# Optimization experiments

Measured on AMD Instinct MI355X. Metric: run time of the kernel, lower is better.

Reference implementation:

```python
import jax, jax.numpy as jnp
import numpy as np
import math

B, T, C, H = 2, 2048, 1024, 16


def setup_inputs() -> dict:
    key = jax.random.key(0)
    k1, k2, k3 = jax.random.split(key, 3)
    x = jax.random.normal(k1, (B, T, C), dtype=jnp.float32)
    qkv_w = jax.random.normal(k2, (3 * C, C), dtype=jnp.float32) * 0.02
    proj_w = jax.random.normal(k3, (C, C), dtype=jnp.float32) * 0.02
    distance_scales = jnp.full((H,), 0.1, dtype=jnp.float32)
    return {"x": x, "qkv_w": qkv_w, "proj_w": proj_w, "distance_scales": distance_scales}


def reference(x, qkv_w, proj_w, distance_scales):
    b, t, c = x.shape
    h = distance_scales.shape[0]
    dh = c // h
    scale = 1.0 / math.sqrt(dh)

    # torch Linear: y = x @ W^T ; split into q, k, v
    qkv = jnp.einsum('btc,oc->bto', x, qkv_w)  # [B,T,3C]
    q, k, v = jnp.split(qkv, 3, axis=-1)
    q = q.reshape(b, t, h, dh).transpose(0, 2, 1, 3)  # [B,H,T,Dh]
    k = k.reshape(b, t, h, dh).transpose(0, 2, 1, 3)
    v = v.reshape(b, t, h, dh).transpose(0, 2, 1, 3)

    logits = jnp.einsum('bhid,bhjd->bhij', q, k) * scale  # [B,H,T,T]

    idx = jnp.arange(t)
    dists = jnp.abs(idx[:, None] - idx[None, :]).astype(x.dtype)  # [T,T]
    logits = logits - distance_scales[None, :, None, None] * dists

    causal = idx[None, :] > idx[:, None]  # True above diagonal -> masked
    logits = jnp.where(causal[None, None, :, :], -jnp.inf, logits)

    attn = jax.nn.softmax(logits, axis=-1)  # [B,H,T,T]

    dist_energy = (attn * dists).sum(axis=-1).mean()
    flop_energy = -(attn * jnp.log(attn + 1e-9)).sum(axis=-1).mean()

    out = jnp.einsum('bhij,bhjd->bhid', attn, v)  # [B,H,T,Dh]
    out = out.transpose(0, 2, 1, 3).reshape(b, t, c)
    out = jnp.einsum('btc,oc->bto', out, proj_w)

    return (out, dist_energy, flop_energy, jax.lax.stop_gradient(attn), jax.lax.stop_gradient(dists))
```

## Files before the change

kernel.cpp:

```cpp
#include <hip/hip_runtime.h>
#include <hip/hip_bf16.h>
#include <math.h>

#define T_SEQ 2048
#define C3 3072
#define C_DIM 1024

typedef __bf16 bf16_t;
typedef __bf16 bf16x8 __attribute__((ext_vector_type(8)));
typedef __bf16 bf16x4_t __attribute__((ext_vector_type(4)));
typedef float f32x4 __attribute__((ext_vector_type(4)));

typedef __attribute__((address_space(1))) const void gconst_t;
typedef __attribute__((address_space(3))) void lds_t;

static __device__ __forceinline__ bf16x8 ldg8(const bf16_t* p) {
    return *reinterpret_cast<const bf16x8*>(p);
}

__global__ void cvt4_kernel(const float* __restrict__ in, bf16_t* __restrict__ out,
                            long n4, float* zbuf) {
    long i = (long)blockIdx.x * blockDim.x + threadIdx.x;
    if (zbuf && i < 2) zbuf[i] = 0.f;
    long stride = (long)gridDim.x * blockDim.x;
    for (; i < n4; i += stride) {
        float4 v = ((const float4*)in)[i];
        bf16x4_t o;
        o[0] = (bf16_t)v.x; o[1] = (bf16_t)v.y; o[2] = (bf16_t)v.z; o[3] = (bf16_t)v.w;
        *(bf16x4_t*)(out + i * 4) = o;
    }
}

__global__ void dists_kernel(float* __restrict__ dout) {
    int idx = blockIdx.x * 256 + threadIdx.x;
    int i = idx >> 11, j = idx & 2047;
    dout[idx] = (float)(i > j ? i - j : j - i);
}

template <int BM, bool OUT_BF16>
__global__ __launch_bounds__(256) void gemm_bt(const bf16_t* __restrict__ A,
                                               const bf16_t* __restrict__ Bw,
                                               void* __restrict__ Cout,
                                               int M, int N, int K) {
    constexpr int WM = BM / 2;
    constexpr int MI = WM / 16;
    __shared__ bf16_t sA[BM * 64];
    __shared__ bf16_t sB[128 * 64];
    int tid = threadIdx.x, lane = tid & 63, wid = tid >> 6;
    int m = lane & 15, quad = lane >> 4;
    int wm = (wid >> 1) * WM, wn = (wid & 1) * 64;
    int m0 = blockIdx.y * BM, n0 = blockIdx.x * 128;
    int lrow = lane >> 3, cxor = (lane & 7) ^ (lrow & 7);

    const bf16_t* Ag = A + (size_t)(m0 + wid * 8 + lrow) * K + cxor * 8;
    const bf16_t* Bg = Bw + (size_t)(n0 + wid * 8 + lrow) * K + cxor * 8;

    f32x4 acc[MI][4] = {};
    for (int k0 = 0; k0 < K; k0 += 64) {
        for (int p = 0; p < BM / 32; ++p)
            __builtin_amdgcn_global_load_lds((gconst_t*)(Ag + (size_t)(p * 32) * K + k0),
                                             (lds_t*)(sA + (p * 32 + wid * 8) * 64), 16, 0, 0);
        for (int p = 0; p < 4; ++p)
            __builtin_amdgcn_global_load_lds((gconst_t*)(Bg + (size_t)(p * 32) * K + k0),
                                             (lds_t*)(sB + (p * 32 + wid * 8) * 64), 16, 0, 0);
        __syncthreads();
        for (int ks = 0; ks < 2; ++ks) {
            bf16x8 a[MI], b[4];
            for (int i = 0; i < MI; ++i) {
                int r = wm + i * 16 + m;
                a[i] = *(const bf16x8*)(sA + r * 64 + ((((ks << 2) + quad) ^ (r & 7)) << 3));
            }
            for (int j = 0; j < 4; ++j) {
                int r = wn + j * 16 + m;
                b[j] = *(const bf16x8*)(sB + r * 64 + ((((ks << 2) + quad) ^ (r & 7)) << 3));
            }
            for (int i = 0; i < MI; ++i)
                for (int j = 0; j < 4; ++j)
                    acc[i][j] = __builtin_amdgcn_mfma_f32_16x16x32_bf16(b[j], a[i], acc[i][j], 0, 0, 0);
        }
        __syncthreads();
    }
    for (int i = 0; i < MI; ++i)
        for (int j = 0; j < 4; ++j) {
            size_t row = m0 + wm + i * 16 + m;
            int col = n0 + wn + j * 16 + quad * 4;
            if (OUT_BF16) {
                bf16x4_t o;
                for (int r = 0; r < 4; ++r) o[r] = (bf16_t)acc[i][j][r];
                *(bf16x4_t*)((bf16_t*)Cout + row * N + col) = o;
            } else {
                *(f32x4*)((float*)Cout + row * N + col) = acc[i][j];
            }
        }
}

__global__ __launch_bounds__(256) void repack_vt(const bf16_t* __restrict__ qkv,
                                                 bf16_t* __restrict__ vt) {
    __shared__ bf16_t s[64][72];
    int t0 = (blockIdx.x & 31) << 6;
    int bh = blockIdx.x >> 5;
    int b = bh >> 4, h = bh & 15;
    int tid = threadIdx.x;
    int r = tid >> 3, c8 = (tid & 7) << 3;
    const bf16_t* src = qkv + (size_t)(b * T_SEQ) * C3 + 2048 + h * 64;
    for (int p = 0; p < 2; ++p) {
        int t = r + p * 32;
        *(uint4*)&s[t][c8] = *(const uint4*)&src[(size_t)(t0 + t) * C3 + c8];
    }
    __syncthreads();
    bf16_t* dst = vt + (size_t)bh * 64 * T_SEQ;
    for (int p = 0; p < 2; ++p) {
        int d = r + p * 32;
        bf16x8 vv;
        for (int i = 0; i < 8; ++i) vv[i] = s[c8 + i][d];
        *(bf16x8*)&dst[(size_t)d * T_SEQ + t0 + c8] = vv;
    }
}

__global__ __launch_bounds__(256) void attn_kernel(const bf16_t* __restrict__ qkv,
                                                   const bf16_t* __restrict__ vt,
                                                   const float* __restrict__ dscales,
                                                   float* __restrict__ attn,
                                                   bf16_t* __restrict__ y,
                                                   float* __restrict__ ews) {
    __shared__ bf16_t sP[64][72];
    __shared__ float sred[8];
    int base = blockIdx.x & 31;
    int bh = blockIdx.x >> 5;
    int it = (bh & 8) ? (31 - base) : base;
    int b = bh >> 4, h = bh & 15;
    int i0 = it << 6;
    int tid = threadIdx.x, lane = tid & 63, wid = tid >> 6;
    int m = lane & 15, quad = lane >> 4;
    int w16 = wid << 4;
    float dsc = dscales[h];
    const float scale = 0.125f;
    const float zthr = 111.0f;

    const bf16_t* Qb = qkv + (size_t)(b * T_SEQ) * C3 + h * 64;
    const bf16_t* Kb = Qb + 1024;
    const bf16_t* Vb = vt + (size_t)bh * 64 * T_SEQ;
    float* Ab = attn + ((size_t)bh * T_SEQ + i0) * T_SEQ;

    {
        int zc0 = i0 + 64, zn = T_SEQ - zc0;
        f32x4 z4 = {0.f, 0.f, 0.f, 0.f};
        for (int r = 0; r < 64; ++r) {
            float* rowp = Ab + (size_t)r * T_SEQ + zc0;
            for (int c = tid << 2; c < zn; c += 1024)
                *(f32x4*)(rowp + c) = z4;
        }
    }

    int i = i0 + w16 + m;
    bf16x8 qf[2];
    qf[0] = ldg8(Qb + (size_t)i * C3 + quad * 8);
    qf[1] = ldg8(Qb + (size_t)i * C3 + 32 + quad * 8);

    float lsum = 0.f;
    for (int jt = 0; jt <= it; ++jt) {
        int j0 = jt << 6;
        if ((float)(i0 - j0 - 63) * dsc > zthr) continue;
        f32x4 acc[4] = {};
        for (int ks = 0; ks < 2; ++ks)
            for (int n = 0; n < 4; ++n) {
                bf16x8 kf = ldg8(Kb + (size_t)(j0 + n * 16 + m) * C3 + ks * 32 + quad * 8);
                acc[n] = __builtin_amdgcn_mfma_f32_16x16x32_bf16(kf, qf[ks], acc[n], 0, 0, 0);
            }
        if (jt < it) {
            for (int n = 0; n < 4; ++n)
                for (int r = 0; r < 4; ++r) {
                    float d = (float)(i - (j0 + n * 16 + quad * 4 + r));
                    lsum += __expf(acc[n][r] * scale - dsc * d);
                }
        } else {
            for (int n = 0; n < 4; ++n)
                for (int r = 0; r < 4; ++r) {
                    int j = j0 + n * 16 + quad * 4 + r;
                    if (j <= i) lsum += __expf(acc[n][r] * scale - dsc * (float)(i - j));
                }
        }
    }
    lsum += __shfl_xor(lsum, 16);
    lsum += __shfl_xor(lsum, 32);
    float rl = 1.f / lsum;

    f32x4 oacc[4] = {};
    float e_d = 0.f, e_e = 0.f;

    for (int jt = 0; jt <= it; ++jt) {
        int j0 = jt << 6;
        if ((float)(i0 - j0 - 63) * dsc > zthr) {
            int rr = tid >> 2, c0 = (tid & 3) << 4;
            float* p0 = Ab + (size_t)rr * T_SEQ + j0 + c0;
            f32x4 z4 = {0.f, 0.f, 0.f, 0.f};
            for (int u = 0; u < 4; ++u) *(f32x4*)(p0 + u * 4) = z4;
            continue;
        }
        f32x4 acc[4] = {};
        for (int ks = 0; ks < 2; ++ks)
            for (int n = 0; n < 4; ++n) {
                bf16x8 kf = ldg8(Kb + (size_t)(j0 + n * 16 + m) * C3 + ks * 32 + quad * 8);
                acc[n] = __builtin_amdgcn_mfma_f32_16x16x32_bf16(kf, qf[ks], acc[n], 0, 0, 0);
            }
        __syncthreads();
        bool diag = (jt == it);
        for (int n = 0; n < 4; ++n) {
            f32x4 pv;
            for (int r = 0; r < 4; ++r) {
                int j = j0 + n * 16 + quad * 4 + r;
                float p = 0.f;
                if (!diag || j <= i) {
                    float d = (float)(i - j);
                    p = __expf(acc[n][r] * scale - dsc * d) * rl;
                    e_d += p * d;
                    e_e += p * __logf(p + 1e-9f);
                }
                pv[r] = p;
            }
            *(f32x4*)(Ab + (size_t)(w16 + m) * T_SEQ + j0 + n * 16 + quad * 4) = pv;
            bf16x4_t pb;
            for (int r = 0; r < 4; ++r) pb[r] = (bf16_t)pv[r];
            *(bf16x4_t*)&sP[w16 + m][n * 16 + quad * 4] = pb;
        }
        __syncthreads();
        for (int ks = 0; ks < 2; ++ks) {
            bf16x8 pf = *(const bf16x8*)&sP[w16 + m][ks * 32 + quad * 8];
            for (int n = 0; n < 4; ++n) {
                bf16x8 vf = ldg8(Vb + (size_t)(n * 16 + m) * T_SEQ + j0 + ks * 32 + quad * 8);
                oacc[n] = __builtin_amdgcn_mfma_f32_16x16x32_bf16(vf, pf, oacc[n], 0, 0, 0);
            }
        }
    }

    for (int n = 0; n < 4; ++n) {
        bf16x4_t o;
        for (int r = 0; r < 4; ++r) o[r] = (bf16_t)oacc[n][r];
        *(bf16x4_t*)(y + (size_t)(b * T_SEQ + i) * C_DIM + h * 64 + n * 16 + quad * 4) = o;
    }

    for (int off = 1; off < 64; off <<= 1) {
        e_d += __shfl_xor(e_d, off);
        e_e += __shfl_xor(e_e, off);
    }
    if (lane == 0) { sred[wid] = e_d; sred[wid + 4] = e_e; }
    __syncthreads();
    if (tid == 0) {
        atomicAdd(ews, sred[0] + sred[1] + sred[2] + sred[3]);
        atomicAdd(ews + 1, sred[4] + sred[5] + sred[6] + sred[7]);
    }
}

__global__ void finalize_kernel(const float* __restrict__ ews, float* __restrict__ dout) {
    dout[4194304] = ews[0] / 65536.f;
    dout[4194305] = -ews[1] / 65536.f;
}

extern "C" void kernel_launch(void* const* d_in, const int* in_sizes, int n_in,
                              void* d_out, int out_size, void* d_ws, size_t ws_size,
                              hipStream_t stream) {
    const float* x = (const float*)d_in[0];
    const float* qkv_w = (const float*)d_in[1];
    const float* proj_w = (const float*)d_in[2];
    const float* dscales = (const float*)d_in[3];
    float* out = (float*)d_out;

    char* ws = (char*)d_ws;
    float* ews   = (float*)ws;
    bf16_t* xb   = (bf16_t*)(ws + 256);
    bf16_t* wb   = xb + 4194304;
    bf16_t* pb   = wb + 3145728;
    bf16_t* qkvb = pb + 1048576;
    bf16_t* vtb  = qkvb + 12582912;
    bf16_t* yb   = vtb + 4194304;

    cvt4_kernel<<<1024, 256, 0, stream>>>(x, xb, 4194304 / 4, ews);
    cvt4_kernel<<<1024, 256, 0, stream>>>(qkv_w, wb, 3145728 / 4, nullptr);
    cvt4_kernel<<<512, 256, 0, stream>>>(proj_w, pb, 1048576 / 4, nullptr);
    dists_kernel<<<16384, 256, 0, stream>>>(out + 138412034);

    gemm_bt<128, true><<<dim3(24, 32), 256, 0, stream>>>(xb, wb, qkvb, 4096, 3072, 1024);
    repack_vt<<<1024, 256, 0, stream>>>(qkvb, vtb);
    attn_kernel<<<1024, 256, 0, stream>>>(qkvb, vtb, dscales, out + 4194306, yb, ews);
    gemm_bt<64, false><<<dim3(8, 64), 256, 0, stream>>>(yb, pb, out, 4096, 1024, 1024);
    finalize_kernel<<<1, 1, 0, stream>>>(ews, out);
}
```

Measured before the change: 873.2 us.

## Fuse prep kernels, tighten distance skip, use nontemporal stores and cheaper entropy

Merges the three fp32-to-bf16 conversion launches and the distance-matrix launch into one kernel. In attention, computes a start tile from the distance scale so that tiles whose probabilities underflow are never visited; their region is bulk-zeroed instead. All attention-matrix and zero writes become nontemporal stores. Entropy is computed as sum p*logit minus log of the row sum, removing a log per element. The tighter threshold drops contributions below roughly exp(-38), which slightly changes numerics.

```diff
diff --git a/kernel.cpp b/kernel.cpp
--- a/kernel.cpp
+++ b/kernel.cpp
@@ -18,23 +18,38 @@
     return *reinterpret_cast<const bf16x8*>(p);
 }
 
-__global__ void cvt4_kernel(const float* __restrict__ in, bf16_t* __restrict__ out,
-                            long n4, float* zbuf) {
-    long i = (long)blockIdx.x * blockDim.x + threadIdx.x;
-    if (zbuf && i < 2) zbuf[i] = 0.f;
-    long stride = (long)gridDim.x * blockDim.x;
-    for (; i < n4; i += stride) {
-        float4 v = ((const float4*)in)[i];
-        bf16x4_t o;
-        o[0] = (bf16_t)v.x; o[1] = (bf16_t)v.y; o[2] = (bf16_t)v.z; o[3] = (bf16_t)v.w;
-        *(bf16x4_t*)(out + i * 4) = o;
-    }
-}
-
-__global__ void dists_kernel(float* __restrict__ dout) {
-    int idx = blockIdx.x * 256 + threadIdx.x;
-    int i = idx >> 11, j = idx & 2047;
-    dout[idx] = (float)(i > j ? i - j : j - i);
+__global__ __launch_bounds__(256) void aux_kernel(const float* __restrict__ x,
+                                                  const float* __restrict__ qw,
+                                                  const float* __restrict__ pw,
+                                                  bf16_t* __restrict__ xb,
+                                                  bf16_t* __restrict__ wb,
+                                                  bf16_t* __restrict__ pb,
+                                                  float* __restrict__ dout,
+                                                  float* __restrict__ ews) {
+    long gid = (long)blockIdx.x * 256 + threadIdx.x;
+    if (gid < 2) ews[gid] = 0.f;
+    const float* src;
+    bf16_t* dst;
+    long u;
+    if (gid < 1048576) { src = x; dst = xb; u = gid; }
+    else if (gid < 1835008) { src = qw; dst = wb; u = gid - 1048576; }
+    else if (gid < 2097152) { src = pw; dst = pb; u = gid - 1835008; }
+    else {
+        long v = gid - 2097152;
+        long e0 = v << 2;
+        int i = (int)(e0 >> 11), j0 = (int)(e0 & 2047);
+        f32x4 o;
+        for (int r = 0; r < 4; ++r) {
+            int j = j0 + r;
+            o[r] = (float)(i > j ? i - j : j - i);
+        }
+        __builtin_nontemporal_store(o, (f32x4*)(dout + e0));
+        return;
+    }
+    float4 v4 = ((const float4*)src)[u];
+    bf16x4_t o;
+    o[0] = (bf16_t)v4.x; o[1] = (bf16_t)v4.y; o[2] = (bf16_t)v4.z; o[3] = (bf16_t)v4.w;
+    *(bf16x4_t*)(dst + u * 4) = o;
 }
 
 template <int BM, bool OUT_BF16>
@@ -135,7 +150,13 @@
     int w16 = wid << 4;
     float dsc = dscales[h];
     const float scale = 0.125f;
-    const float zthr = 111.0f;
+
+    int jskip = 0;
+    if (dsc > 1e-6f) {
+        int keep = (int)(38.0f / dsc + 63.0f) >> 6;
+        jskip = it - keep;
+        if (jskip < 0) jskip = 0;
+    }
 
     const bf16_t* Qb = qkv + (size_t)(b * T_SEQ) * C3 + h * 64;
     const bf16_t* Kb = Qb + 1024;
@@ -143,12 +164,18 @@
     float* Ab = attn + ((size_t)bh * T_SEQ + i0) * T_SEQ;
 
     {
+        f32x4 z4 = {0.f, 0.f, 0.f, 0.f};
+        int ln = jskip << 6;
+        for (int r = 0; r < 64; ++r) {
+            float* rowp = Ab + (size_t)r * T_SEQ;
+            for (int c = tid << 2; c < ln; c += 1024)
+                __builtin_nontemporal_store(z4, (f32x4*)(rowp + c));
+        }
         int zc0 = i0 + 64, zn = T_SEQ - zc0;
-        f32x4 z4 = {0.f, 0.f, 0.f, 0.f};
         for (int r = 0; r < 64; ++r) {
             float* rowp = Ab + (size_t)r * T_SEQ + zc0;
             for (int c = tid << 2; c < zn; c += 1024)
-                *(f32x4*)(rowp + c) = z4;
+                __builtin_nontemporal_store(z4, (f32x4*)(rowp + c));
         }
     }
 
@@ -158,9 +185,8 @@
     qf[1] = ldg8(Qb + (size_t)i * C3 + 32 + quad * 8);
 
     float lsum = 0.f;
-    for (int jt = 0; jt <= it; ++jt) {
+    for (int jt = jskip; jt <= it; ++jt) {
         int j0 = jt << 6;
-        if ((float)(i0 - j0 - 63) * dsc > zthr) continue;
         f32x4 acc[4] = {};
         for (int ks = 0; ks < 2; ++ks)
             for (int n = 0; n < 4; ++n) {
@@ -186,17 +212,11 @@
     float rl = 1.f / lsum;
 
     f32x4 oacc[4] = {};
-    float e_d = 0.f, e_e = 0.f;
-
-    for (int jt = 0; jt <= it; ++jt) {
+    float e_d = 0.f;
+    float e_e = (quad == 0) ? -__logf(lsum) : 0.f;
+
+    for (int jt = jskip; jt <= it; ++jt) {
         int j0 = jt << 6;
-        if ((float)(i0 - j0 - 63) * dsc > zthr) {
-            int rr = tid >> 2, c0 = (tid & 3) << 4;
-            float* p0 = Ab + (size_t)rr * T_SEQ + j0 + c0;
-            f32x4 z4 = {0.f, 0.f, 0.f, 0.f};
-            for (int u = 0; u < 4; ++u) *(f32x4*)(p0 + u * 4) = z4;
-            continue;
-        }
         f32x4 acc[4] = {};
         for (int ks = 0; ks < 2; ++ks)
             for (int n = 0; n < 4; ++n) {
@@ -212,13 +232,15 @@
                 float p = 0.f;
                 if (!diag || j <= i) {
                     float d = (float)(i - j);
-                    p = __expf(acc[n][r] * scale - dsc * d) * rl;
+                    float v = acc[n][r] * scale - dsc * d;
+                    p = __expf(v) * rl;
                     e_d += p * d;
-                    e_e += p * __logf(p + 1e-9f);
+                    e_e += p * v;
                 }
                 pv[r] = p;
             }
-            *(f32x4*)(Ab + (size_t)(w16 + m) * T_SEQ + j0 + n * 16 + quad * 4) = pv;
+            __builtin_nontemporal_store(
+                pv, (f32x4*)(Ab + (size_t)(w16 + m) * T_SEQ + j0 + n * 16 + quad * 4));
             bf16x4_t pb;
             for (int r = 0; r < 4; ++r) pb[r] = (bf16_t)pv[r];
             *(bf16x4_t*)&sP[w16 + m][n * 16 + quad * 4] = pb;
@@ -274,11 +296,8 @@
     bf16_t* vtb  = qkvb + 12582912;
     bf16_t* yb   = vtb + 4194304;
 
-    cvt4_kernel<<<1024, 256, 0, stream>>>(x, xb, 4194304 / 4, ews);
-    cvt4_kernel<<<1024, 256, 0, stream>>>(qkv_w, wb, 3145728 / 4, nullptr);
-    cvt4_kernel<<<512, 256, 0, stream>>>(proj_w, pb, 1048576 / 4, nullptr);
-    dists_kernel<<<16384, 256, 0, stream>>>(out + 138412034);
-
+    aux_kernel<<<12288, 256, 0, stream>>>(x, qkv_w, proj_w, xb, wb, pb,
+                                          out + 138412034, ews);
     gemm_bt<128, true><<<dim3(24, 32), 256, 0, stream>>>(xb, wb, qkvb, 4096, 3072, 1024);
     repack_vt<<<1024, 256, 0, stream>>>(qkvb, vtb);
     attn_kernel<<<1024, 256, 0, stream>>>(qkvb, vtb, dscales, out + 4194306, yb, ews);
```

Measured after the change: 850.4 us. 2.6% less time.
